# Optimization experiments

Measured on AMD Instinct MI355X. Metric: run time of the kernel, lower is better.

The kernel has to match this reference:

```python
import jax, jax.numpy as jnp
import numpy as np

D = 768
HEAD_SIZE = 64  # D // 12


def setup_inputs() -> dict:
    key = jax.random.key(0)
    k_ix, k_wk, k_wq, k_wv = jax.random.split(key, 4)
    ix = jax.random.normal(k_ix, (4, 4096, D), dtype=jnp.float32)
    s = 1.0 / np.sqrt(D)
    Wk = jax.random.normal(k_wk, (D, HEAD_SIZE), dtype=jnp.float32) * s
    Wq = jax.random.normal(k_wq, (D, HEAD_SIZE), dtype=jnp.float32) * s
    Wv = jax.random.normal(k_wv, (D, HEAD_SIZE), dtype=jnp.float32) * s
    return {"ix": ix, "Wk": Wk, "Wq": Wq, "Wv": Wv}


def reference(ix, Wk, Wq, Wv):
    # ix: [B, N, D]; W*: [D, h]
    k = ix @ Wk            # [B, N, h]
    q = ix @ Wq            # [B, N, h]
    v = ix @ Wv            # [B, N, h]
    scale = HEAD_SIZE ** -0.5
    wei = jnp.einsum('bnh,bmh->bnm', q, k) * scale  # [B, N, N]
    wei = jax.nn.softmax(wei, axis=-1)
    out = jnp.einsum('bnm,bmh->bnh', wei, v)        # [B, N, h]
    return out
```

## Files before the change

### kernel.cpp

```cpp
#include <hip/hip_runtime.h>
#include <math.h>

#define Dm   768
#define Hm   64
#define SEQ  4096
#define NB   4
#define NROW (NB * SEQ)

#define QSCALE (0.125f * 1.4426950408889634f)

typedef _Float16 f16;
typedef __attribute__((ext_vector_type(8))) _Float16 f16x8;
typedef __attribute__((ext_vector_type(2))) __fp16 fp16x2_raw;
typedef __attribute__((ext_vector_type(4))) float f32x4;
typedef unsigned int uint;
typedef unsigned short ushort;

#define MFMAH(A, B, C) __builtin_amdgcn_mfma_f32_16x16x32_f16(A, B, C, 0, 0, 0)

__device__ __forceinline__ uint pkrtz(float a, float b) {
    fp16x2_raw r = __builtin_amdgcn_cvt_pkrtz(a, b);
    return __builtin_bit_cast(uint, r);
}
__device__ __forceinline__ ushort f2h(float f) {
    f16 h = (f16)f;
    return __builtin_bit_cast(ushort, h);
}
union F16x8U { uint u[4]; f16x8 v; };

__global__ __launch_bounds__(256) void wconv(
    const float* __restrict__ Wq, const float* __restrict__ Wk,
    const float* __restrict__ Wv, ushort* __restrict__ WTt)
{
    __shared__ ushort lt[64 * 33];
    const int b  = blockIdx.x;
    const int kt = b / 3, m = b - kt * 3;
    const float* W = (m == 0) ? Wq : (m == 1 ? Wk : Wv);
    const float sc = (m == 0) ? QSCALE : 1.0f;
    const int t = threadIdx.x;
#pragma unroll
    for (int p = 0; p < 8; ++p) {
        int t2 = p * 256 + t;
        int kl = t2 >> 6, c = t2 & 63;
        lt[c * 33 + kl] = f2h(W[(size_t)(kt * 32 + kl) * 64 + c] * sc);
    }
    __syncthreads();
#pragma unroll
    for (int p = 0; p < 8; ++p) {
        int t2 = p * 256 + t;
        int c = t2 >> 5, kk = t2 & 31;
        WTt[((size_t)kt * 192 + m * 64 + c) * 32 + kk] = lt[c * 33 + kk];
    }
}

__global__ __launch_bounds__(256, 2) void proj(
    const float* __restrict__ ix, const ushort* __restrict__ WTt,
    ushort* __restrict__ Qw, ushort* __restrict__ Kt, ushort* __restrict__ Vt)
{
    __shared__ __align__(16) float comb[2][2][3072];

    const int t    = threadIdx.x;
    const int lane = t & 63;
    const int kh   = __builtin_amdgcn_readfirstlane(t >> 6);
    const int q15  = lane & 15, quad = lane >> 4;
    const int gr0  = blockIdx.x * 32;

    const float* Ab0 = ix + (size_t)(gr0 + q15) * Dm + kh * 192 + quad * 8;
    const float* Ab1 = Ab0 + (size_t)16 * Dm;
    const ushort* Bb = WTt + ((size_t)(kh * 6) * 192 + q15) * 32 + quad * 8;

    f32x4 acc[2][12];
#pragma unroll
    for (int rt = 0; rt < 2; ++rt)
#pragma unroll
        for (int ct = 0; ct < 12; ++ct) acc[rt][ct] = (f32x4){0.f, 0.f, 0.f, 0.f};

    f32x4 Af[2][3][2];
#pragma unroll
    for (int i = 0; i < 2; ++i) {
        Af[0][i][0] = *(const f32x4*)(Ab0 + i * 32);
        Af[0][i][1] = *(const f32x4*)(Ab0 + i * 32 + 4);
        Af[1][i][0] = *(const f32x4*)(Ab1 + i * 32);
        Af[1][i][1] = *(const f32x4*)(Ab1 + i * 32 + 4);
    }

#pragma unroll
    for (int it = 0; it < 6; ++it) {
        f16x8 Bf[12];
#pragma unroll
        for (int ct = 0; ct < 12; ++ct)
            Bf[ct] = *(const f16x8*)(Bb + (size_t)it * 6144 + ct * 512);

        if (it + 2 < 6) {
            Af[0][(it + 2) % 3][0] = *(const f32x4*)(Ab0 + (it + 2) * 32);
            Af[0][(it + 2) % 3][1] = *(const f32x4*)(Ab0 + (it + 2) * 32 + 4);
            Af[1][(it + 2) % 3][0] = *(const f32x4*)(Ab1 + (it + 2) * 32);
            Af[1][(it + 2) % 3][1] = *(const f32x4*)(Ab1 + (it + 2) * 32 + 4);
        }

        F16x8U af0, af1;
        af0.u[0] = pkrtz(Af[0][it % 3][0].x, Af[0][it % 3][0].y);
        af0.u[1] = pkrtz(Af[0][it % 3][0].z, Af[0][it % 3][0].w);
        af0.u[2] = pkrtz(Af[0][it % 3][1].x, Af[0][it % 3][1].y);
        af0.u[3] = pkrtz(Af[0][it % 3][1].z, Af[0][it % 3][1].w);
        af1.u[0] = pkrtz(Af[1][it % 3][0].x, Af[1][it % 3][0].y);
        af1.u[1] = pkrtz(Af[1][it % 3][0].z, Af[1][it % 3][0].w);
        af1.u[2] = pkrtz(Af[1][it % 3][1].x, Af[1][it % 3][1].y);
        af1.u[3] = pkrtz(Af[1][it % 3][1].z, Af[1][it % 3][1].w);
        __builtin_amdgcn_s_setprio(1);
#pragma unroll
        for (int ct = 0; ct < 12; ++ct) {
            acc[0][ct] = MFMAH(af0.v, Bf[ct], acc[0][ct]);
            acc[1][ct] = MFMAH(af1.v, Bf[ct], acc[1][ct]);
        }
        __builtin_amdgcn_s_setprio(0);
    }

    if (kh >= 2) {
#pragma unroll
        for (int rt = 0; rt < 2; ++rt)
#pragma unroll
            for (int ct = 0; ct < 12; ++ct)
                *(f32x4*)&comb[rt][kh - 2][(ct * 64 + lane) * 4] = acc[rt][ct];
    }
    __syncthreads();
    if (kh < 2) {
#pragma unroll
        for (int rt = 0; rt < 2; ++rt)
#pragma unroll
            for (int ct = 0; ct < 12; ++ct) {
                f32x4 o = *(const f32x4*)&comb[rt][kh][(ct * 64 + lane) * 4];
                acc[rt][ct].x += o.x; acc[rt][ct].y += o.y;
                acc[rt][ct].z += o.z; acc[rt][ct].w += o.w;
            }
    }
    __syncthreads();
    if (kh == 1) {
#pragma unroll
        for (int rt = 0; rt < 2; ++rt)
#pragma unroll
            for (int ct = 0; ct < 12; ++ct)
                *(f32x4*)&comb[rt][0][(ct * 64 + lane) * 4] = acc[rt][ct];
    }
    __syncthreads();
    if (kh == 0) {
#pragma unroll
        for (int rt = 0; rt < 2; ++rt) {
#pragma unroll
            for (int ct = 0; ct < 12; ++ct) {
                f32x4 o = *(const f32x4*)&comb[rt][0][(ct * 64 + lane) * 4];
                acc[rt][ct].x += o.x; acc[rt][ct].y += o.y;
                acc[rt][ct].z += o.z; acc[rt][ct].w += o.w;
            }
            const int gr  = gr0 + rt * 16;
            const int n4  = gr >> 4;
            const int h16 = n4 & 1;
            const int j32 = gr >> 5;
#pragma unroll
            for (int ct = 0; ct < 12; ++ct) {
                float vals[4] = {acc[rt][ct].x, acc[rt][ct].y, acc[rt][ct].z, acc[rt][ct].w};
                if (ct < 4) {
#pragma unroll
                    for (int r = 0; r < 4; ++r)
                        Qw[(size_t)(gr + quad * 4 + r) * 64 + ct * 16 + q15] = f2h(vals[r]);
                } else if (ct < 8) {
#pragma unroll
                    for (int r = 0; r < 4; ++r)
                        Kt[(size_t)n4 * 1024 + (ct - 4) * 256 + (quad * 4 + r) * 16 + q15] = f2h(vals[r]);
                } else {
                    ushort4 vv;
                    vv.x = f2h(vals[0]); vv.y = f2h(vals[1]);
                    vv.z = f2h(vals[2]); vv.w = f2h(vals[3]);
                    *(ushort4*)(Vt + (size_t)j32 * 2048 + (ct - 8) * 512 +
                                (h16 * 2 + (quad >> 1)) * 128 + q15 * 8 + (quad & 1) * 4) = vv;
                }
            }
        }
    }
}

#define OSTR 68
#define OBUF 4352

__global__ __launch_bounds__(512, 2) void attn(
    const ushort* __restrict__ Qw, const ushort* __restrict__ Kt,
    const ushort* __restrict__ Vt, float* __restrict__ out)
{
    __shared__ __align__(16) float aF[20992];
    short* aS = (short*)aF;

    const int t    = threadIdx.x;
    const int lane = t & 63;
    const int w    = __builtin_amdgcn_readfirstlane(t >> 6);
    const int q15  = lane & 15, quad = lane >> 4;

    const int bb    = blockIdx.x;
    const int xcd   = bb & 7;
    const int batch = xcd >> 1;
    const int slot  = (bb >> 3) | ((xcd & 1) << 5);
    const int q0    = slot * 64;
    const size_t base = (size_t)batch * SEQ;

    f16x8 qf[4][2];
#pragma unroll
    for (int g = 0; g < 4; ++g)
#pragma unroll
        for (int h = 0; h < 2; ++h)
            qf[g][h] = *(const f16x8*)(Qw + (base + q0 + g * 16 + q15) * 64 + h * 32 + quad * 8);

    f32x4 oacc[4][4];
#pragma unroll
    for (int g = 0; g < 4; ++g)
#pragma unroll
        for (int dt = 0; dt < 4; ++dt) oacc[g][dt] = (f32x4){0.f, 0.f, 0.f, 0.f};
    float lsum[4] = {0.f, 0.f, 0.f, 0.f};

    const size_t j0g = base + w * 512;
    const ushort* Kfb = Kt + (j0g >> 4) * 1024;
    const ushort* Vfb = Vt + (j0g >> 5) * 2048 + lane * 8;
    short* Ps = aS + w * 5120;

    int koff[2][2];
#pragma unroll
    for (int jt = 0; jt < 2; ++jt)
#pragma unroll
        for (int h = 0; h < 2; ++h)
            koff[jt][h] = jt * 1024 + h * 512 + (quad >> 1) * 256 + q15 * 16 + (quad & 1) * 8;

    f16x8 kf[3][2][2], vf[3][4];

#define LOADKV(slotc, i)                                                       \
    {                                                                          \
        _Pragma("unroll") for (int jt = 0; jt < 2; ++jt)                       \
        _Pragma("unroll") for (int h = 0; h < 2; ++h)                          \
            kf[slotc][jt][h] = *(const f16x8*)(Kfb + (size_t)(i) * 2048 + koff[jt][h]); \
        _Pragma("unroll") for (int dt = 0; dt < 4; ++dt)                       \
            vf[slotc][dt] = *(const f16x8*)(Vfb + (size_t)(i) * 2048 + dt * 512); \
    }
#define QKSTEP(slotc, pb)                                                      \
    {                                                                          \
        _Pragma("unroll") for (int g = 0; g < 4; ++g)                          \
        _Pragma("unroll") for (int jt = 0; jt < 2; ++jt) {                     \
            f32x4 z = (f32x4){0.f, 0.f, 0.f, 0.f};                             \
            z = MFMAH(kf[slotc][jt][0], qf[g][0], z);                          \
            z = MFMAH(kf[slotc][jt][1], qf[g][1], z);                          \
            float e0 = exp2f(z.x), e1 = exp2f(z.y);                            \
            float e2 = exp2f(z.z), e3 = exp2f(z.w);                            \
            lsum[g] += (e0 + e1) + (e2 + e3);                                  \
            uint2 pk = make_uint2(pkrtz(e0, e1), pkrtz(e2, e3));               \
            *(uint2*)(Ps + (pb) * 2560 + (g * 16 + q15) * 40 + jt * 16 + quad * 4) = pk; \
        }                                                                      \
    }
#define PVSTEP(slotc, pb)                                                      \
    {                                                                          \
        f16x8 pf[4];                                                           \
        _Pragma("unroll") for (int g = 0; g < 4; ++g)                          \
            pf[g] = *(const f16x8*)(Ps + (pb) * 2560 + (g * 16 + q15) * 40 + quad * 8); \
        __builtin_amdgcn_s_setprio(1);                                         \
        _Pragma("unroll") for (int dt = 0; dt < 4; ++dt)                       \
        _Pragma("unroll") for (int g = 0; g < 4; ++g)                          \
            oacc[g][dt] = MFMAH(pf[g], vf[slotc][dt], oacc[g][dt]);            \
        __builtin_amdgcn_s_setprio(0);                                         \
    }

    LOADKV(0, 0);
    LOADKV(1, 1);
    QKSTEP(0, 0);
#pragma unroll
    for (int i = 0; i < 16; ++i) {
        if (i + 2 < 16) LOADKV((i + 2) % 3, i + 2);
        if (i + 1 < 16) QKSTEP((i + 1) % 3, (i + 1) & 1);
        PVSTEP(i % 3, i & 1);
    }

#pragma unroll
    for (int g = 0; g < 4; ++g) {
        lsum[g] += __shfl_xor(lsum[g], 16);
        lsum[g] += __shfl_xor(lsum[g], 32);
    }
    if (quad == 0) {
#pragma unroll
        for (int g = 0; g < 4; ++g)
            aF[20480 + w * 64 + g * 16 + q15] = lsum[g];
    }
    __syncthreads();

#define OWRITE(idx)                                                          \
    {                                                                        \
        float* b = aF + (idx) * OBUF;                                        \
        _Pragma("unroll") for (int g = 0; g < 4; ++g)                        \
        _Pragma("unroll") for (int dt = 0; dt < 4; ++dt) {                   \
            b[(g * 16 + quad * 4 + 0) * OSTR + dt * 16 + q15] = oacc[g][dt].x; \
            b[(g * 16 + quad * 4 + 1) * OSTR + dt * 16 + q15] = oacc[g][dt].y; \
            b[(g * 16 + quad * 4 + 2) * OSTR + dt * 16 + q15] = oacc[g][dt].z; \
            b[(g * 16 + quad * 4 + 3) * OSTR + dt * 16 + q15] = oacc[g][dt].w; \
        }                                                                    \
    }
#define OADD(idx)                                                            \
    {                                                                        \
        const float* b = aF + (idx) * OBUF;                                  \
        _Pragma("unroll") for (int g = 0; g < 4; ++g)                        \
        _Pragma("unroll") for (int dt = 0; dt < 4; ++dt) {                   \
            oacc[g][dt].x += b[(g * 16 + quad * 4 + 0) * OSTR + dt * 16 + q15];\
            oacc[g][dt].y += b[(g * 16 + quad * 4 + 1) * OSTR + dt * 16 + q15];\
            oacc[g][dt].z += b[(g * 16 + quad * 4 + 2) * OSTR + dt * 16 + q15];\
            oacc[g][dt].w += b[(g * 16 + quad * 4 + 3) * OSTR + dt * 16 + q15];\
        }                                                                    \
    }
    if (w >= 4) OWRITE(w - 4);
    __syncthreads();
    if (w < 4) OADD(w);
    __syncthreads();
    if (w == 2 || w == 3) OWRITE(w - 2);
    __syncthreads();
    if (w < 2) OADD(w);
    __syncthreads();
    if (w < 2) OWRITE(w);
    __syncthreads();

    {
        const int q  = t >> 3;
        const int d0 = (t & 7) * 8;
        float l = 0.f;
#pragma unroll
        for (int i = 0; i < 8; ++i) l += aF[20480 + i * 64 + q];
        const float linv = 1.0f / l;
#pragma unroll
        for (int k2 = 0; k2 < 2; ++k2) {
            float4 a = *(const float4*)&aF[q * OSTR + d0 + k2 * 4];
            float4 b = *(const float4*)&aF[OBUF + q * OSTR + d0 + k2 * 4];
            float4 s;
            s.x = (a.x + b.x) * linv; s.y = (a.y + b.y) * linv;
            s.z = (a.z + b.z) * linv; s.w = (a.w + b.w) * linv;
            *(float4*)(out + (base + q0 + q) * 64 + d0 + k2 * 4) = s;
        }
    }
}

extern "C" void kernel_launch(void* const* d_in, const int* in_sizes, int n_in,
                              void* d_out, int out_size, void* d_ws, size_t ws_size,
                              hipStream_t stream)
{
    const float* ix = (const float*)d_in[0];
    const float* Wk = (const float*)d_in[1];
    const float* Wq = (const float*)d_in[2];
    const float* Wv = (const float*)d_in[3];
    float* out = (float*)d_out;

    ushort* Qw  = (ushort*)d_ws;
    ushort* Kt  = Qw + (size_t)NROW * Hm;
    ushort* Vt  = Kt + (size_t)NROW * Hm;
    ushort* WTt = Vt + (size_t)NROW * Hm;

    wconv<<<72, 256, 0, stream>>>(Wq, Wk, Wv, WTt);
    proj<<<512, 256, 0, stream>>>(ix, WTt, Qw, Kt, Vt);
    attn<<<256, 512, 0, stream>>>(Qw, Kt, Vt, out);
}
```

Before: 128.9 us.

## Split QK and softmax stages to batch MFMAs and shrink K/V buffering

Splits the fused QK-matmul+exp step into separate matmul and softmax-pack stages, and reorders the per-iteration schedule so the QK MFMAs for the next block and the PV MFMAs for the current block run back-to-back under raised priority, with exp/pack work afterwards. K/V register buffering drops from three slots to two, and the next load is issued after the matmuls. The aim is denser MFMA issue and lower register pressure. The trade-off is less load latency hiding, since global loads now get only about one iteration of lead.

```diff
diff --git a/kernel.cpp b/kernel.cpp
--- a/kernel.cpp
+++ b/kernel.cpp
@@ -227,7 +227,9 @@
         for (int h = 0; h < 2; ++h)
             koff[jt][h] = jt * 1024 + h * 512 + (quad >> 1) * 256 + q15 * 16 + (quad & 1) * 8;
 
-    f16x8 kf[3][2][2], vf[3][4];
+    f16x8 kf[2][2][2], vf[2][4];
+    f32x4 zz[4][2];
+    f16x8 pf[4];
 
 #define LOADKV(slotc, i)                                                       \
     {                                                                          \
@@ -237,40 +239,52 @@
         _Pragma("unroll") for (int dt = 0; dt < 4; ++dt)                       \
             vf[slotc][dt] = *(const f16x8*)(Vfb + (size_t)(i) * 2048 + dt * 512); \
     }
-#define QKSTEP(slotc, pb)                                                      \
+#define QKMM(slotc)                                                            \
     {                                                                          \
         _Pragma("unroll") for (int g = 0; g < 4; ++g)                          \
         _Pragma("unroll") for (int jt = 0; jt < 2; ++jt) {                     \
             f32x4 z = (f32x4){0.f, 0.f, 0.f, 0.f};                             \
             z = MFMAH(kf[slotc][jt][0], qf[g][0], z);                          \
             z = MFMAH(kf[slotc][jt][1], qf[g][1], z);                          \
-            float e0 = exp2f(z.x), e1 = exp2f(z.y);                            \
-            float e2 = exp2f(z.z), e3 = exp2f(z.w);                            \
+            zz[g][jt] = z;                                                     \
+        }                                                                      \
+    }
+#define SMPACK(pb)                                                             \
+    {                                                                          \
+        _Pragma("unroll") for (int g = 0; g < 4; ++g)                          \
+        _Pragma("unroll") for (int jt = 0; jt < 2; ++jt) {                     \
+            float e0 = exp2f(zz[g][jt].x), e1 = exp2f(zz[g][jt].y);            \
+            float e2 = exp2f(zz[g][jt].z), e3 = exp2f(zz[g][jt].w);            \
             lsum[g] += (e0 + e1) + (e2 + e3);                                  \
             uint2 pk = make_uint2(pkrtz(e0, e1), pkrtz(e2, e3));               \
             *(uint2*)(Ps + (pb) * 2560 + (g * 16 + q15) * 40 + jt * 16 + quad * 4) = pk; \
         }                                                                      \
     }
-#define PVSTEP(slotc, pb)                                                      \
-    {                                                                          \
-        f16x8 pf[4];                                                           \
+#define PFLOAD(pb)                                                             \
+    {                                                                          \
         _Pragma("unroll") for (int g = 0; g < 4; ++g)                          \
             pf[g] = *(const f16x8*)(Ps + (pb) * 2560 + (g * 16 + q15) * 40 + quad * 8); \
-        __builtin_amdgcn_s_setprio(1);                                         \
+    }
+#define PVMM(slotc)                                                            \
+    {                                                                          \
         _Pragma("unroll") for (int dt = 0; dt < 4; ++dt)                       \
         _Pragma("unroll") for (int g = 0; g < 4; ++g)                          \
             oacc[g][dt] = MFMAH(pf[g], vf[slotc][dt], oacc[g][dt]);            \
-        __builtin_amdgcn_s_setprio(0);                                         \
     }
 
     LOADKV(0, 0);
     LOADKV(1, 1);
-    QKSTEP(0, 0);
+    QKMM(0);
+    SMPACK(0);
 #pragma unroll
     for (int i = 0; i < 16; ++i) {
-        if (i + 2 < 16) LOADKV((i + 2) % 3, i + 2);
-        if (i + 1 < 16) QKSTEP((i + 1) % 3, (i + 1) & 1);
-        PVSTEP(i % 3, i & 1);
+        PFLOAD(i & 1);
+        __builtin_amdgcn_s_setprio(1);
+        if (i + 1 < 16) QKMM((i + 1) & 1);
+        PVMM(i & 1);
+        __builtin_amdgcn_s_setprio(0);
+        if (i + 2 < 16) LOADKV(i & 1, i + 2);
+        if (i + 1 < 16) SMPACK((i + 1) & 1);
     }
 
 #pragma unroll
```

Result: no change. 128.0 us (-0.8%).
